# Performance work log

Hardware: AMD Instinct MI355X
Metric: run time of the kernel (lower is better)

## Reference

```python
import jax, jax.numpy as jnp
import numpy as np

TAU = 0.07
EPS = 1e-12  # matches torch F.normalize clamp_min eps


def setup_inputs() -> dict:
    key = jax.random.key(0)
    k1, k2 = jax.random.split(key)
    feat = jax.random.normal(k1, (4, 64, 512, 512), dtype=jnp.float32)
    gt = jax.random.randint(k2, (4, 19, 512, 512), 0, 2, dtype=jnp.int32)
    return {"feat": feat, "gt": gt}


def reference(feat, gt):
    # feat: [b, c, h, w], gt: [b, k, h, w] multi-hot in {0,1}
    mask = (gt == 1).astype(feat.dtype)                      # [b,k,h,w]
    num_pos = mask.sum()

    # Scatter-sum class prototypes: k0[k] = sum of feat at positive pixels of class k
    k0 = jnp.einsum('bkhw,bchw->kc', mask, feat)             # [k,c]
    k0n = k0 / jnp.maximum(jnp.linalg.norm(k0, axis=1, keepdims=True), EPS)

    # Per-pixel L2-normalized features over channel dim
    fn = feat / jnp.maximum(jnp.linalg.norm(feat, axis=1, keepdims=True), EPS)

    # Cosine similarity to every prototype, temperature-scaled softmax NLL over classes
    logits = jnp.einsum('kc,bchw->bkhw', k0n, fn) / TAU      # [b,k,h,w]
    logp = jax.nn.log_softmax(logits, axis=1)

    # Sum NLL over all (pixel, class) positive pairs; a pixel positive for
    # multiple classes contributes once per class, exactly like the loop.
    loss = -(mask * logp).sum() / num_pos
    return loss
```

## Files before the change

kernel.cpp:

```cpp
#include <hip/hip_runtime.h>
#include <cstdint>
#include <cstddef>

#define HW    262144
#define C     64
#define K     19
#define NPIX  1048576
#define TAUINV (1.0f / 0.07f)
#define EPS   1e-12f

#define NCHUNK (NPIX / 32)
#define CPB    8192
#define G1     1024


typedef __attribute__((ext_vector_type(8))) short bf16x8;
typedef __attribute__((ext_vector_type(4))) float f32x4;

__device__ __forceinline__ float wave_reduce_f32(float v) {
#pragma unroll
    for (int off = 32; off; off >>= 1) v += __shfl_down(v, off);
    return v;
}
__device__ __forceinline__ unsigned wave_reduce_u32(unsigned v) {
#pragma unroll
    for (int off = 32; off; off >>= 1) v += __shfl_down(v, off);
    return v;
}

__device__ __forceinline__ void split1(float f, short& h, short& l) {
    const unsigned u  = __float_as_uint(f);
    const unsigned hb = (u + 0x7FFFu + ((u >> 16) & 1u)) & 0xFFFF0000u;
    h = (short)(hb >> 16);
    const float lo = f - __uint_as_float(hb);
    const unsigned v = __float_as_uint(lo);
    l = (short)((v + 0x7FFFu + ((v >> 16) & 1u)) >> 16);
}

__global__ __launch_bounds__(256) void k1_proto(
    const float* __restrict__ feat, const int* __restrict__ gt,
    unsigned* __restrict__ pm,
    float* __restrict__ k0p, unsigned* __restrict__ num_pos)
{
    __shared__ float red[32 * 64];
    const int tid  = threadIdx.x;
    const int lane = tid & 63;
    const int wv   = tid >> 6;
    const int q    = lane >> 4;
    const int n    = lane & 15;
    const int q8   = q << 3;

    f32x4 acc[2][4];
#pragma unroll
    for (int mt = 0; mt < 2; ++mt)
#pragma unroll
        for (int nt = 0; nt < 4; ++nt)
            acc[mt][nt] = (f32x4){0.f, 0.f, 0.f, 0.f};
    unsigned npos = 0;

    const int wave_id = blockIdx.x * 4 + wv;
    const int nwaves  = G1 * 4;

    for (int chunk = wave_id; chunk < NCHUNK; chunk += nwaves) {
        const int b   = chunk >> 13;
        const int hw0 = (chunk & (CPB - 1)) << 5;
        const size_t fbase = (size_t)b * C * HW + hw0;

        unsigned mymask = 0;
        if (lane < 32) {
            const int* gp = gt + (size_t)b * K * HW + hw0 + lane;
#pragma unroll
            for (int k = 0; k < K; ++k)
                mymask |= (gp[(size_t)k * HW] == 1) ? (1u << k) : 0u;
            pm[(size_t)chunk * 32 + lane] = mymask;
            npos += __popc(mymask);
        }

        unsigned w8[8];
#pragma unroll
        for (int j = 0; j < 8; ++j) w8[j] = __shfl(mymask, q8 + j);
        bf16x8 a0, a1;
#pragma unroll
        for (int j = 0; j < 8; ++j) {
            a0[j] = (short)(((w8[j] >> n) & 1u) * 0x3F80u);
            a1[j] = (short)(((w8[j] >> (n + 16)) & 1u) * 0x3F80u);
        }

        const float* fp = feat + fbase + (size_t)n * HW + q8;
#pragma unroll
        for (int nt = 0; nt < 4; ++nt) {
            const float* p = fp + (size_t)(nt * 16) * HW;
            const float4 x = *(const float4*)p;
            const float4 y = *(const float4*)(p + 4);
            bf16x8 bh, bl;
            {
                short h, l;
                split1(x.x, h, l); bh[0] = h; bl[0] = l;
                split1(x.y, h, l); bh[1] = h; bl[1] = l;
                split1(x.z, h, l); bh[2] = h; bl[2] = l;
                split1(x.w, h, l); bh[3] = h; bl[3] = l;
                split1(y.x, h, l); bh[4] = h; bl[4] = l;
                split1(y.y, h, l); bh[5] = h; bl[5] = l;
                split1(y.z, h, l); bh[6] = h; bl[6] = l;
                split1(y.w, h, l); bh[7] = h; bl[7] = l;
            }
            acc[0][nt] = __builtin_amdgcn_mfma_f32_16x16x32_bf16(a0, bh, acc[0][nt], 0, 0, 0);
            acc[0][nt] = __builtin_amdgcn_mfma_f32_16x16x32_bf16(a0, bl, acc[0][nt], 0, 0, 0);
            acc[1][nt] = __builtin_amdgcn_mfma_f32_16x16x32_bf16(a1, bh, acc[1][nt], 0, 0, 0);
            acc[1][nt] = __builtin_amdgcn_mfma_f32_16x16x32_bf16(a1, bl, acc[1][nt], 0, 0, 0);
        }
    }

    for (int w = 0; w < 4; ++w) {
        if (wv == w) {
#pragma unroll
            for (int mt = 0; mt < 2; ++mt)
#pragma unroll
                for (int nt = 0; nt < 4; ++nt)
#pragma unroll
                    for (int r = 0; r < 4; ++r) {
                        const int idx = (mt * 16 + q * 4 + r) * 64 + nt * 16 + n;
                        if (w == 0) red[idx]  = acc[mt][nt][r];
                        else        red[idx] += acc[mt][nt][r];
                    }
        }
        __syncthreads();
    }
    for (int i = tid; i < 32 * 64; i += 256)
        atomicAdd(&k0p[i], red[i]);

    const unsigned np = wave_reduce_u32(npos);
    if (lane == 0) atomicAdd(num_pos, np);
}

__global__ __launch_bounds__(256) void k2_norm(
    const float* __restrict__ k0p, float* __restrict__ k0n)
{
    __shared__ float rn[K];
    const int tid  = threadIdx.x;
    const int lane = tid & 63;
    const int wv   = tid >> 6;
    for (int cls = wv; cls < K; cls += 4) {
        const float v = k0p[cls * 64 + lane];
        const float s = wave_reduce_f32(v * v);
        if (lane == 0) rn[cls] = 1.0f / fmaxf(sqrtf(s), EPS);
    }
    __syncthreads();
    for (int i = tid; i < K * 64; i += 256) k0n[i] = k0p[i] * rn[i >> 6];
}

__global__ __launch_bounds__(256) void k3_loss(
    const float* __restrict__ feat, const int* __restrict__ gt,
    const unsigned* __restrict__ pm, const float* __restrict__ k0n,
    float* __restrict__ loss_sum)
{
    __shared__ __align__(16) float w[K * 64];
    const int tid = threadIdx.x;
    for (int i = tid; i < K * 64; i += 256) w[i] = k0n[i];
    __syncthreads();

    const int px0 = (blockIdx.x * 256 + tid) << 2;
    const int b   = px0 >> 18;
    const int hw  = px0 & (HW - 1);
    const float* fb = feat + (size_t)b * C * HW + hw;

    unsigned marr[4];
    {
        const uint4 mv = *(const uint4*)(pm + px0);
        marr[0] = mv.x; marr[1] = mv.y; marr[2] = mv.z; marr[3] = mv.w;
    }

    float4 dot[K];
#pragma unroll
    for (int k = 0; k < K; ++k) dot[k] = make_float4(0.f, 0.f, 0.f, 0.f);
    float4 ss = make_float4(0.f, 0.f, 0.f, 0.f);

    float4 f[8];
#pragma unroll
    for (int j = 0; j < 8; ++j)
        f[j] = *(const float4*)(fb + (size_t)j * HW);

#pragma unroll
    for (int cg = 0; cg < 64; cg += 8) {
        float4 g[8];
        if (cg + 8 < 64) {
#pragma unroll
            for (int j = 0; j < 8; ++j)
                g[j] = *(const float4*)(fb + (size_t)(cg + 8 + j) * HW);
        }
#pragma unroll
        for (int j = 0; j < 8; ++j) {
            const float4 fv = f[j];
            ss.x = fmaf(fv.x, fv.x, ss.x); ss.y = fmaf(fv.y, fv.y, ss.y);
            ss.z = fmaf(fv.z, fv.z, ss.z); ss.w = fmaf(fv.w, fv.w, ss.w);
        }
#pragma unroll
        for (int k = 0; k < K; ++k) {
            const float4 wa = *(const float4*)&w[k * 64 + cg];
            const float4 wb = *(const float4*)&w[k * 64 + cg + 4];
            float4 d = dot[k];
            d.x = fmaf(f[0].x, wa.x, d.x); d.y = fmaf(f[0].y, wa.x, d.y);
            d.z = fmaf(f[0].z, wa.x, d.z); d.w = fmaf(f[0].w, wa.x, d.w);
            d.x = fmaf(f[1].x, wa.y, d.x); d.y = fmaf(f[1].y, wa.y, d.y);
            d.z = fmaf(f[1].z, wa.y, d.z); d.w = fmaf(f[1].w, wa.y, d.w);
            d.x = fmaf(f[2].x, wa.z, d.x); d.y = fmaf(f[2].y, wa.z, d.y);
            d.z = fmaf(f[2].z, wa.z, d.z); d.w = fmaf(f[2].w, wa.z, d.w);
            d.x = fmaf(f[3].x, wa.w, d.x); d.y = fmaf(f[3].y, wa.w, d.y);
            d.z = fmaf(f[3].z, wa.w, d.z); d.w = fmaf(f[3].w, wa.w, d.w);
            d.x = fmaf(f[4].x, wb.x, d.x); d.y = fmaf(f[4].y, wb.x, d.y);
            d.z = fmaf(f[4].z, wb.x, d.z); d.w = fmaf(f[4].w, wb.x, d.w);
            d.x = fmaf(f[5].x, wb.y, d.x); d.y = fmaf(f[5].y, wb.y, d.y);
            d.z = fmaf(f[5].z, wb.y, d.z); d.w = fmaf(f[5].w, wb.y, d.w);
            d.x = fmaf(f[6].x, wb.z, d.x); d.y = fmaf(f[6].y, wb.z, d.y);
            d.z = fmaf(f[6].z, wb.z, d.z); d.w = fmaf(f[6].w, wb.z, d.w);
            d.x = fmaf(f[7].x, wb.w, d.x); d.y = fmaf(f[7].y, wb.w, d.y);
            d.z = fmaf(f[7].z, wb.w, d.z); d.w = fmaf(f[7].w, wb.w, d.w);
            dot[k] = d;
        }
        if (cg + 8 < 64) {
#pragma unroll
            for (int j = 0; j < 8; ++j) f[j] = g[j];
        }
    }

    float ls = 0.0f;
    float* dp = (float*)&dot[0];
    const float* sp = (const float*)&ss;
#pragma unroll
    for (int comp = 0; comp < 4; ++comp) {
        const float sc = TAUINV / fmaxf(sqrtf(sp[comp]), EPS);
        float mx = -1e30f;
#pragma unroll
        for (int k = 0; k < K; ++k) {
            dp[k * 4 + comp] *= sc;
            mx = fmaxf(mx, dp[k * 4 + comp]);
        }
        float se = 0.0f;
#pragma unroll
        for (int k = 0; k < K; ++k) se += expf(dp[k * 4 + comp] - mx);
        const float logZ = mx + logf(se);
        const unsigned m = marr[comp];
        ls += (float)__popc(m) * logZ;
#pragma unroll
        for (int k = 0; k < K; ++k) {
            const int s = ((int)(m << (31 - k))) >> 31;
            ls -= __int_as_float(s & __float_as_int(dp[k * 4 + comp]));
        }
    }

    ls = wave_reduce_f32(ls);
    if ((tid & 63) == 0) atomicAdd(loss_sum, ls);
}

__global__ void k4_final(const float* __restrict__ loss_sum,
                         const unsigned* __restrict__ num_pos,
                         float* __restrict__ out)
{
    out[0] = loss_sum[0] / (float)num_pos[0];
}

extern "C" void kernel_launch(void* const* d_in, const int* in_sizes, int n_in,
                              void* d_out, int out_size, void* d_ws, size_t ws_size,
                              hipStream_t stream)
{
    const float* feat = (const float*)d_in[0];
    const int*   gt   = (const int*)d_in[1];
    float*       out  = (float*)d_out;

    char* ws = (char*)d_ws;
    unsigned* num_pos  = (unsigned*)(ws + 0);
    float*    loss_sum = (float*)(ws + 4);
    float*    k0p      = (float*)(ws + 256);
    float*    k0n      = (float*)(ws + 8448);
    unsigned* pm       = (unsigned*)(ws + 65536);

    hipMemsetAsync(d_ws, 0, 16384, stream);

    k1_proto<<<G1, 256, 0, stream>>>(feat, gt, pm, k0p, num_pos);
    k2_norm <<<1,  256, 0, stream>>>(k0p, k0n);
    k3_loss <<<NPIX / 1024, 256, 0, stream>>>(feat, gt, pm, k0n, loss_sum);
    k4_final<<<1, 1, 0, stream>>>(loss_sum, num_pos, out);
}
```

Measured before the change: 536.5 us.

## Split mask packing into separate kernel and restructure prototype and loss kernels

Mask bit-packing and the positive count move into a new kernel that reads gt with int4 vector loads. The prototype kernel then only streams feat plus the packed mask. It now processes 64 pixels per wave across all four batches, prefetches feat in registers, and splits to bf16 with packed hardware conversion. The loss kernel handles 2 pixels per thread instead of 4, which lowers register pressure and doubles the grid. The trade-off is an extra launch and an extra pass over the packed mask, in exchange for better memory-level parallelism and occupancy.

```diff
diff --git a/kernel.cpp b/kernel.cpp
--- a/kernel.cpp
+++ b/kernel.cpp
@@ -1,4 +1,5 @@
 #include <hip/hip_runtime.h>
+#include <hip/hip_bf16.h>
 #include <cstdint>
 #include <cstddef>
 
@@ -9,10 +10,6 @@
 #define TAUINV (1.0f / 0.07f)
 #define EPS   1e-12f
 
-#define NCHUNK (NPIX / 32)
-#define CPB    8192
-#define G1     1024
-
 
 typedef __attribute__((ext_vector_type(8))) short bf16x8;
 typedef __attribute__((ext_vector_type(4))) float f32x4;
@@ -28,19 +25,58 @@
     return v;
 }
 
-__device__ __forceinline__ void split1(float f, short& h, short& l) {
-    const unsigned u  = __float_as_uint(f);
-    const unsigned hb = (u + 0x7FFFu + ((u >> 16) & 1u)) & 0xFFFF0000u;
-    h = (short)(hb >> 16);
-    const float lo = f - __uint_as_float(hb);
-    const unsigned v = __float_as_uint(lo);
-    l = (short)((v + 0x7FFFu + ((v >> 16) & 1u)) >> 16);
-}
-
-__global__ __launch_bounds__(256) void k1_proto(
-    const float* __restrict__ feat, const int* __restrict__ gt,
-    unsigned* __restrict__ pm,
-    float* __restrict__ k0p, unsigned* __restrict__ num_pos)
+__device__ __forceinline__ short2 pk_bf16(float a, float b) {
+    union { __hip_bfloat162 bf; short2 s; } u;
+    u.bf = __float22bfloat162_rn(make_float2(a, b));
+    return u.s;
+}
+__device__ __forceinline__ float bf2f(short s) {
+    return __uint_as_float((unsigned)(unsigned short)s << 16);
+}
+
+__device__ __forceinline__ void split8(const float4 x, const float4 y,
+                                       bf16x8& h, bf16x8& l) {
+    const short2 h01 = pk_bf16(x.x, x.y), h23 = pk_bf16(x.z, x.w);
+    const short2 h45 = pk_bf16(y.x, y.y), h67 = pk_bf16(y.z, y.w);
+    const short2 l01 = pk_bf16(x.x - bf2f(h01.x), x.y - bf2f(h01.y));
+    const short2 l23 = pk_bf16(x.z - bf2f(h23.x), x.w - bf2f(h23.y));
+    const short2 l45 = pk_bf16(y.x - bf2f(h45.x), y.y - bf2f(h45.y));
+    const short2 l67 = pk_bf16(y.z - bf2f(h67.x), y.w - bf2f(h67.y));
+    h[0] = h01.x; h[1] = h01.y; h[2] = h23.x; h[3] = h23.y;
+    h[4] = h45.x; h[5] = h45.y; h[6] = h67.x; h[7] = h67.y;
+    l[0] = l01.x; l[1] = l01.y; l[2] = l23.x; l[3] = l23.y;
+    l[4] = l45.x; l[5] = l45.y; l[6] = l67.x; l[7] = l67.y;
+}
+
+__global__ __launch_bounds__(256) void k0_mask(
+    const int* __restrict__ gt, unsigned* __restrict__ pm,
+    unsigned* __restrict__ num_pos)
+{
+    const int g   = blockIdx.x * 256 + threadIdx.x;
+    const int px0 = g << 2;
+    const int b   = px0 >> 18;
+    const int hw  = px0 & (HW - 1);
+    const int* gp = gt + (size_t)b * K * HW + hw;
+
+    unsigned m0 = 0, m1 = 0, m2 = 0, m3 = 0;
+#pragma unroll
+    for (int k = 0; k < K; ++k) {
+        const int4 gv = *(const int4*)(gp + (size_t)k * HW);
+        m0 |= (gv.x == 1) ? (1u << k) : 0u;
+        m1 |= (gv.y == 1) ? (1u << k) : 0u;
+        m2 |= (gv.z == 1) ? (1u << k) : 0u;
+        m3 |= (gv.w == 1) ? (1u << k) : 0u;
+    }
+    *(uint4*)(pm + px0) = make_uint4(m0, m1, m2, m3);
+
+    unsigned np = __popc(m0) + __popc(m1) + __popc(m2) + __popc(m3);
+    np = wave_reduce_u32(np);
+    if ((threadIdx.x & 63) == 0) atomicAdd(num_pos, np);
+}
+
+__global__ __launch_bounds__(256, 3) void k1_proto(
+    const float* __restrict__ feat, const unsigned* __restrict__ pm,
+    float* __restrict__ k0p)
 {
     __shared__ float red[32 * 64];
     const int tid  = threadIdx.x;
@@ -49,6 +85,7 @@
     const int q    = lane >> 4;
     const int n    = lane & 15;
     const int q8   = q << 3;
+    const int wave_id = blockIdx.x * 4 + wv;
 
     f32x4 acc[2][4];
 #pragma unroll
@@ -56,58 +93,60 @@
 #pragma unroll
         for (int nt = 0; nt < 4; ++nt)
             acc[mt][nt] = (f32x4){0.f, 0.f, 0.f, 0.f};
-    unsigned npos = 0;
-
-    const int wave_id = blockIdx.x * 4 + wv;
-    const int nwaves  = G1 * 4;
-
-    for (int chunk = wave_id; chunk < NCHUNK; chunk += nwaves) {
-        const int b   = chunk >> 13;
-        const int hw0 = (chunk & (CPB - 1)) << 5;
-        const size_t fbase = (size_t)b * C * HW + hw0;
-
-        unsigned mymask = 0;
-        if (lane < 32) {
-            const int* gp = gt + (size_t)b * K * HW + hw0 + lane;
-#pragma unroll
-            for (int k = 0; k < K; ++k)
-                mymask |= (gp[(size_t)k * HW] == 1) ? (1u << k) : 0u;
-            pm[(size_t)chunk * 32 + lane] = mymask;
-            npos += __popc(mymask);
-        }
-
-        unsigned w8[8];
-#pragma unroll
-        for (int j = 0; j < 8; ++j) w8[j] = __shfl(mymask, q8 + j);
-        bf16x8 a0, a1;
-#pragma unroll
-        for (int j = 0; j < 8; ++j) {
-            a0[j] = (short)(((w8[j] >> n) & 1u) * 0x3F80u);
-            a1[j] = (short)(((w8[j] >> (n + 16)) & 1u) * 0x3F80u);
-        }
-
-        const float* fp = feat + fbase + (size_t)n * HW + q8;
+
+    const int hw0 = wave_id << 6;
+    const float* fb = feat + (size_t)hw0 + (size_t)n * HW + q8;
+    const unsigned* pmp = pm + (size_t)wave_id * 64 + lane;
+
+    float4   F[16];
+    unsigned mreg;
+
+#pragma unroll
+    for (int nt = 0; nt < 4; ++nt)
+#pragma unroll
+        for (int kh = 0; kh < 2; ++kh) {
+            const float* p = fb + (size_t)(nt * 16) * HW + kh * 32;
+            F[nt * 4 + kh * 2 + 0] = *(const float4*)p;
+            F[nt * 4 + kh * 2 + 1] = *(const float4*)(p + 4);
+        }
+    mreg = *pmp;
+
+#pragma unroll
+    for (int j = 0; j < 4; ++j) {
+        bf16x8 A[2][2];
+#pragma unroll
+        for (int jj = 0; jj < 8; ++jj) {
+            const unsigned ma = __shfl(mreg, q8 + jj);
+            const unsigned mb = __shfl(mreg, 32 + q8 + jj);
+            A[0][0][jj] = (short)(((ma >> n) & 1u) * 0x3F80u);
+            A[0][1][jj] = (short)(((ma >> (n + 16)) & 1u) * 0x3F80u);
+            A[1][0][jj] = (short)(((mb >> n) & 1u) * 0x3F80u);
+            A[1][1][jj] = (short)(((mb >> (n + 16)) & 1u) * 0x3F80u);
+        }
+        if (j < 3) mreg = pmp[(j + 1) * (NPIX / 4)];
+        const float* fbn = fb + (size_t)(j + 1) * C * HW;
+
 #pragma unroll
         for (int nt = 0; nt < 4; ++nt) {
-            const float* p = fp + (size_t)(nt * 16) * HW;
-            const float4 x = *(const float4*)p;
-            const float4 y = *(const float4*)(p + 4);
-            bf16x8 bh, bl;
-            {
-                short h, l;
-                split1(x.x, h, l); bh[0] = h; bl[0] = l;
-                split1(x.y, h, l); bh[1] = h; bl[1] = l;
-                split1(x.z, h, l); bh[2] = h; bl[2] = l;
-                split1(x.w, h, l); bh[3] = h; bl[3] = l;
-                split1(y.x, h, l); bh[4] = h; bl[4] = l;
-                split1(y.y, h, l); bh[5] = h; bl[5] = l;
-                split1(y.z, h, l); bh[6] = h; bl[6] = l;
-                split1(y.w, h, l); bh[7] = h; bl[7] = l;
+            bf16x8 BH0, BL0, BH1, BL1;
+            split8(F[nt * 4 + 0], F[nt * 4 + 1], BH0, BL0);
+            split8(F[nt * 4 + 2], F[nt * 4 + 3], BH1, BL1);
+            if (j < 3) {
+#pragma unroll
+                for (int kh = 0; kh < 2; ++kh) {
+                    const float* p = fbn + (size_t)(nt * 16) * HW + kh * 32;
+                    F[nt * 4 + kh * 2 + 0] = *(const float4*)p;
+                    F[nt * 4 + kh * 2 + 1] = *(const float4*)(p + 4);
+                }
             }
-            acc[0][nt] = __builtin_amdgcn_mfma_f32_16x16x32_bf16(a0, bh, acc[0][nt], 0, 0, 0);
-            acc[0][nt] = __builtin_amdgcn_mfma_f32_16x16x32_bf16(a0, bl, acc[0][nt], 0, 0, 0);
-            acc[1][nt] = __builtin_amdgcn_mfma_f32_16x16x32_bf16(a1, bh, acc[1][nt], 0, 0, 0);
-            acc[1][nt] = __builtin_amdgcn_mfma_f32_16x16x32_bf16(a1, bl, acc[1][nt], 0, 0, 0);
+            acc[0][nt] = __builtin_amdgcn_mfma_f32_16x16x32_bf16(A[0][0], BH0, acc[0][nt], 0, 0, 0);
+            acc[1][nt] = __builtin_amdgcn_mfma_f32_16x16x32_bf16(A[0][1], BH0, acc[1][nt], 0, 0, 0);
+            acc[0][nt] = __builtin_amdgcn_mfma_f32_16x16x32_bf16(A[0][0], BL0, acc[0][nt], 0, 0, 0);
+            acc[1][nt] = __builtin_amdgcn_mfma_f32_16x16x32_bf16(A[0][1], BL0, acc[1][nt], 0, 0, 0);
+            acc[0][nt] = __builtin_amdgcn_mfma_f32_16x16x32_bf16(A[1][0], BH1, acc[0][nt], 0, 0, 0);
+            acc[1][nt] = __builtin_amdgcn_mfma_f32_16x16x32_bf16(A[1][1], BH1, acc[1][nt], 0, 0, 0);
+            acc[0][nt] = __builtin_amdgcn_mfma_f32_16x16x32_bf16(A[1][0], BL1, acc[0][nt], 0, 0, 0);
+            acc[1][nt] = __builtin_amdgcn_mfma_f32_16x16x32_bf16(A[1][1], BL1, acc[1][nt], 0, 0, 0);
         }
     }
 
@@ -128,9 +167,6 @@
     }
     for (int i = tid; i < 32 * 64; i += 256)
         atomicAdd(&k0p[i], red[i]);
-
-    const unsigned np = wave_reduce_u32(npos);
-    if (lane == 0) atomicAdd(num_pos, np);
 }
 
 __global__ __launch_bounds__(256) void k2_norm(
@@ -150,101 +186,89 @@
 }
 
 __global__ __launch_bounds__(256) void k3_loss(
-    const float* __restrict__ feat, const int* __restrict__ gt,
-    const unsigned* __restrict__ pm, const float* __restrict__ k0n,
-    float* __restrict__ loss_sum)
+    const float* __restrict__ feat, const unsigned* __restrict__ pm,
+    const float* __restrict__ k0n, float* __restrict__ loss_sum)
 {
     __shared__ __align__(16) float w[K * 64];
     const int tid = threadIdx.x;
     for (int i = tid; i < K * 64; i += 256) w[i] = k0n[i];
     __syncthreads();
 
-    const int px0 = (blockIdx.x * 256 + tid) << 2;
+    const int g   = blockIdx.x * 256 + tid;
+    const int px0 = g << 1;
     const int b   = px0 >> 18;
     const int hw  = px0 & (HW - 1);
     const float* fb = feat + (size_t)b * C * HW + hw;
 
-    unsigned marr[4];
-    {
-        const uint4 mv = *(const uint4*)(pm + px0);
-        marr[0] = mv.x; marr[1] = mv.y; marr[2] = mv.z; marr[3] = mv.w;
-    }
-
-    float4 dot[K];
-#pragma unroll
-    for (int k = 0; k < K; ++k) dot[k] = make_float4(0.f, 0.f, 0.f, 0.f);
-    float4 ss = make_float4(0.f, 0.f, 0.f, 0.f);
-
-    float4 f[8];
+    const uint2 mv = *(const uint2*)(pm + px0);
+
+    float2 dot[K];
+#pragma unroll
+    for (int k = 0; k < K; ++k) dot[k] = make_float2(0.f, 0.f);
+    float2 ss = make_float2(0.f, 0.f);
+
+    float2 f[8];
 #pragma unroll
     for (int j = 0; j < 8; ++j)
-        f[j] = *(const float4*)(fb + (size_t)j * HW);
+        f[j] = *(const float2*)(fb + (size_t)j * HW);
 
 #pragma unroll
     for (int cg = 0; cg < 64; cg += 8) {
-        float4 g[8];
+        float2 gq[8];
         if (cg + 8 < 64) {
 #pragma unroll
             for (int j = 0; j < 8; ++j)
-                g[j] = *(const float4*)(fb + (size_t)(cg + 8 + j) * HW);
+                gq[j] = *(const float2*)(fb + (size_t)(cg + 8 + j) * HW);
         }
 #pragma unroll
         for (int j = 0; j < 8; ++j) {
-            const float4 fv = f[j];
-            ss.x = fmaf(fv.x, fv.x, ss.x); ss.y = fmaf(fv.y, fv.y, ss.y);
-            ss.z = fmaf(fv.z, fv.z, ss.z); ss.w = fmaf(fv.w, fv.w, ss.w);
+            ss.x = fmaf(f[j].x, f[j].x, ss.x);
+            ss.y = fmaf(f[j].y, f[j].y, ss.y);
         }
 #pragma unroll
         for (int k = 0; k < K; ++k) {
             const float4 wa = *(const float4*)&w[k * 64 + cg];
             const float4 wb = *(const float4*)&w[k * 64 + cg + 4];
-            float4 d = dot[k];
+            float2 d = dot[k];
             d.x = fmaf(f[0].x, wa.x, d.x); d.y = fmaf(f[0].y, wa.x, d.y);
-            d.z = fmaf(f[0].z, wa.x, d.z); d.w = fmaf(f[0].w, wa.x, d.w);
             d.x = fmaf(f[1].x, wa.y, d.x); d.y = fmaf(f[1].y, wa.y, d.y);
-            d.z = fmaf(f[1].z, wa.y, d.z); d.w = fmaf(f[1].w, wa.y, d.w);
             d.x = fmaf(f[2].x, wa.z, d.x); d.y = fmaf(f[2].y, wa.z, d.y);
-            d.z = fmaf(f[2].z, wa.z, d.z); d.w = fmaf(f[2].w, wa.z, d.w);
             d.x = fmaf(f[3].x, wa.w, d.x); d.y = fmaf(f[3].y, wa.w, d.y);
-            d.z = fmaf(f[3].z, wa.w, d.z); d.w = fmaf(f[3].w, wa.w, d.w);
             d.x = fmaf(f[4].x, wb.x, d.x); d.y = fmaf(f[4].y, wb.x, d.y);
-            d.z = fmaf(f[4].z, wb.x, d.z); d.w = fmaf(f[4].w, wb.x, d.w);
             d.x = fmaf(f[5].x, wb.y, d.x); d.y = fmaf(f[5].y, wb.y, d.y);
-            d.z = fmaf(f[5].z, wb.y, d.z); d.w = fmaf(f[5].w, wb.y, d.w);
             d.x = fmaf(f[6].x, wb.z, d.x); d.y = fmaf(f[6].y, wb.z, d.y);
-            d.z = fmaf(f[6].z, wb.z, d.z); d.w = fmaf(f[6].w, wb.z, d.w);
             d.x = fmaf(f[7].x, wb.w, d.x); d.y = fmaf(f[7].y, wb.w, d.y);
-            d.z = fmaf(f[7].z, wb.w, d.z); d.w = fmaf(f[7].w, wb.w, d.w);
             dot[k] = d;
         }
         if (cg + 8 < 64) {
 #pragma unroll
-            for (int j = 0; j < 8; ++j) f[j] = g[j];
+            for (int j = 0; j < 8; ++j) f[j] = gq[j];
         }
     }
 
     float ls = 0.0f;
     float* dp = (float*)&dot[0];
-    const float* sp = (const float*)&ss;
-#pragma unroll
-    for (int comp = 0; comp < 4; ++comp) {
-        const float sc = TAUINV / fmaxf(sqrtf(sp[comp]), EPS);
+    const float sarr[2] = {ss.x, ss.y};
+    const unsigned marr[2] = {mv.x, mv.y};
+#pragma unroll
+    for (int comp = 0; comp < 2; ++comp) {
+        const float sc = TAUINV / fmaxf(sqrtf(sarr[comp]), EPS);
         float mx = -1e30f;
 #pragma unroll
         for (int k = 0; k < K; ++k) {
-            dp[k * 4 + comp] *= sc;
-            mx = fmaxf(mx, dp[k * 4 + comp]);
+            dp[k * 2 + comp] *= sc;
+            mx = fmaxf(mx, dp[k * 2 + comp]);
         }
         float se = 0.0f;
 #pragma unroll
-        for (int k = 0; k < K; ++k) se += expf(dp[k * 4 + comp] - mx);
+        for (int k = 0; k < K; ++k) se += expf(dp[k * 2 + comp] - mx);
         const float logZ = mx + logf(se);
         const unsigned m = marr[comp];
         ls += (float)__popc(m) * logZ;
 #pragma unroll
         for (int k = 0; k < K; ++k) {
             const int s = ((int)(m << (31 - k))) >> 31;
-            ls -= __int_as_float(s & __float_as_int(dp[k * 4 + comp]));
+            ls -= __int_as_float(s & __float_as_int(dp[k * 2 + comp]));
         }
     }
 
@@ -276,8 +300,9 @@
 
     hipMemsetAsync(d_ws, 0, 16384, stream);
 
-    k1_proto<<<G1, 256, 0, stream>>>(feat, gt, pm, k0p, num_pos);
-    k2_norm <<<1,  256, 0, stream>>>(k0p, k0n);
-    k3_loss <<<NPIX / 1024, 256, 0, stream>>>(feat, gt, pm, k0n, loss_sum);
+    k0_mask<<<NPIX / 1024, 256, 0, stream>>>(gt, pm, num_pos);
+    k1_proto<<<1024,       256, 0, stream>>>(feat, pm, k0p);
+    k2_norm <<<1,          256, 0, stream>>>(k0p, k0n);
+    k3_loss <<<NPIX / 512, 256, 0, stream>>>(feat, pm, k0n, loss_sum);
     k4_final<<<1, 1, 0, stream>>>(loss_sum, num_pos, out);
 }
```

New measurement: 587.4 us. +9.5%, slower.
